# Kernel optimization log

Hardware: AMD Instinct MI355X
Metric: run time of the kernel (lower is better)

## Reference

```python
import jax, jax.numpy as jnp
import numpy as np

UNITS = 256  # LSTM hidden size per source (units=256)

def setup_inputs() -> dict:
    key = jax.random.key(0)
    ks = jax.random.split(key, 7)
    vocab, embed_dim, seq_len, batch, n_cls = 50000, 256, 512, 64, 20
    x = jax.random.randint(ks[0], (batch, seq_len), 0, vocab)
    emb = jax.random.normal(ks[1], (vocab, embed_dim), jnp.float32) * 0.05
    W = jax.random.normal(ks[2], (embed_dim, 4 * UNITS), jnp.float32) * (1.0 / np.sqrt(embed_dim))
    U = jax.random.normal(ks[3], (UNITS, 4 * UNITS), jnp.float32) * (1.0 / np.sqrt(UNITS))
    # keras unit_forget_bias: forget-gate bias = 1, others 0 (gate order i,f,c,o)
    b = jnp.concatenate([jnp.zeros((UNITS,)), jnp.ones((UNITS,)), jnp.zeros((2 * UNITS,))]).astype(jnp.float32)
    Wd = jax.random.normal(ks[4], (UNITS, n_cls), jnp.float32) * (1.0 / np.sqrt(UNITS))
    bd = jnp.zeros((n_cls,), jnp.float32)
    return {"x": x, "emb": emb, "W": W, "U": U, "b": b, "Wd": Wd, "bd": bd}

def reference(x, emb, W, U, b, Wd, bd):
    # Embedding lookup: [B, T] -> [B, T, D]
    e = emb[x]
    B = e.shape[0]
    # Pre-compute input projections for all timesteps (one big GEMM): [B, T, 4H]
    xz = jnp.einsum('btd,dh->bth', e, W) + b
    h0 = jnp.zeros((B, UNITS), e.dtype)
    c0 = jnp.zeros((B, UNITS), e.dtype)

    def step(carry, zt):
        h, c = carry
        z = zt + h @ U  # [B, 4H]
        i, f, g, o = jnp.split(z, 4, axis=-1)
        i = jax.nn.sigmoid(i)
        f = jax.nn.sigmoid(f)
        g = jnp.tanh(g)
        o = jax.nn.sigmoid(o)
        c_new = f * c + i * g
        h_new = o * jnp.tanh(c_new)
        return (h_new, c_new), None

    (h_T, _), _ = jax.lax.scan(step, (h0, c0), jnp.swapaxes(xz, 0, 1))
    logits = h_T @ Wd + bd
    return jax.nn.softmax(logits, axis=-1)
```

## Files before the change

### kernel.cpp

```cpp
#include <hip/hip_runtime.h>
#include <hip/hip_bf16.h>
#include <math.h>


typedef __bf16 bf16_t;
typedef bf16_t bf16x8 __attribute__((ext_vector_type(8)));
typedef bf16_t bf16x4 __attribute__((ext_vector_type(4)));
typedef float  f32x4  __attribute__((ext_vector_type(4)));
typedef unsigned long long u64;

#define T_SZ 512
#define HID 256
#define G4 1024
#define NCLS 20

#define WS_UPACK 0u
#define WS_WPACK (512u * 1024u)
#define WS_HFIN  (1024u * 1024u)
#define WS_EXCH  (1536u * 1024u)
#define WS_XZ    (2u * 1024u * 1024u)

__global__ void pack_weights(const float* __restrict__ W, const float* __restrict__ U,
                             bf16_t* __restrict__ Wp, bf16_t* __restrict__ Up) {
    int tid  = blockIdx.x * blockDim.x + threadIdx.x;
    int j    = tid & 7;
    int lane = (tid >> 3) & 63;
    int ks   = (tid >> 9) & 7;
    int nt   = tid >> 12;
    int row  = ks * 32 + ((lane >> 4) << 3) + j;
    int col  = nt * 16 + (lane & 15);
    Wp[tid] = (bf16_t)W[row * G4 + col];
    Up[tid] = (bf16_t)U[row * G4 + col];
}

__global__ __launch_bounds__(256) void xz_gemm(const int* __restrict__ x,
                                               const float* __restrict__ emb,
                                               const bf16_t* __restrict__ Wp,
                                               const float* __restrict__ bias,
                                               bf16x4* __restrict__ xz2) {
    int nb   = blockIdx.x & 7;
    int t    = blockIdx.x >> 3;
    int w    = threadIdx.x >> 6;
    int lane = threadIdx.x & 63;
    int l15  = lane & 15;
    int quad = lane >> 4;

    int b_row = w * 16 + l15;
    int tok   = x[b_row * T_SZ + t];
    const float* erow = emb + (size_t)tok * 256;

    bf16x8 afrag[8];
#pragma unroll
    for (int ks = 0; ks < 8; ks++) {
        const float4* p = (const float4*)(erow + ks * 32 + quad * 8);
        float4 v0 = p[0], v1 = p[1];
        bf16x8 a;
        a[0] = (bf16_t)v0.x; a[1] = (bf16_t)v0.y; a[2] = (bf16_t)v0.z; a[3] = (bf16_t)v0.w;
        a[4] = (bf16_t)v1.x; a[5] = (bf16_t)v1.y; a[6] = (bf16_t)v1.z; a[7] = (bf16_t)v1.w;
        afrag[ks] = a;
    }

    const bf16x8* Wf = (const bf16x8*)Wp;

#pragma unroll
    for (int nt = 0; nt < 8; nt++) {
        int ntg = nb * 8 + nt;
        float bv = bias[ntg * 16 + l15];
        f32x4 acc = {bv, bv, bv, bv};
        const bf16x8* bp = Wf + (size_t)(ntg * 8) * 64 + lane;
#pragma unroll
        for (int ks = 0; ks < 8; ks++) {
            bf16x8 bfrag = bp[ks * 64];
            acc = __builtin_amdgcn_mfma_f32_16x16x32_bf16(afrag[ks], bfrag, acc, 0, 0, 0);
        }
        bf16x4 hv;
#pragma unroll
        for (int r = 0; r < 4; r++) hv[r] = (bf16_t)acc[r];
        xz2[((size_t)(t * 4 + w) * 64 + ntg) * 64 + lane] = hv;
    }
}

__device__ __forceinline__ float sigmoid_f(float z) {
    return 1.0f / (1.0f + __expf(-z));
}
__device__ __forceinline__ float tanh_f(float z) {
    float e = __expf(2.0f * z);
    return 1.0f - 2.0f / (e + 1.0f);
}
__device__ __forceinline__ unsigned pack2(float a, float b) {
    unsigned short xs = __builtin_bit_cast(unsigned short, (bf16_t)a);
    unsigned short ys = __builtin_bit_cast(unsigned short, (bf16_t)b);
    return (unsigned)xs | ((unsigned)ys << 16);
}
__device__ __forceinline__ bf16_t unpk_lo(unsigned v) {
    return __builtin_bit_cast(bf16_t, (unsigned short)(v & 0xffffu));
}
__device__ __forceinline__ bf16_t unpk_hi(unsigned v) {
    return __builtin_bit_cast(bf16_t, (unsigned short)(v >> 16));
}

__device__ __forceinline__ void mfma_aB(f32x4& d, bf16x8 a, bf16x8 b) {
    asm("v_mfma_f32_16x16x32_bf16 %0, %1, %2, %0" : "+v"(d) : "v"(a), "a"(b));
}

__global__ __launch_bounds__(512, 2) void lstm_pair(const bf16x4* __restrict__ xz2,
                                                    const bf16_t* __restrict__ Up,
                                                    u64* __restrict__ exch,
                                                    float* __restrict__ hfin) {
    if (blockIdx.x & 4) return;
    const int g    = blockIdx.x & 3;
    const int p    = (blockIdx.x >> 3) & 1;
    const int w    = threadIdx.x >> 6;
    const int lane = threadIdx.x & 63;
    const int l15  = lane & 15;
    const int quad = lane >> 4;

    __shared__ __align__(16) bf16_t h_lds[2][16][264];

    const bf16x8* Uf = (const bf16x8*)Up + lane;
    bf16x8 u[4][8];
#pragma unroll
    for (int G = 0; G < 4; G++) {
        int ntg = G * 16 + p * 8 + w;
#pragma unroll
        for (int ks = 0; ks < 8; ks++)
            u[G][ks] = Uf[(ntg * 8 + ks) * 64];
    }
    asm volatile("" : "+a"(u[0][0]), "+a"(u[0][1]), "+a"(u[0][2]), "+a"(u[0][3]),
                      "+a"(u[0][4]), "+a"(u[0][5]), "+a"(u[0][6]), "+a"(u[0][7]));
    asm volatile("" : "+a"(u[1][0]), "+a"(u[1][1]), "+a"(u[1][2]), "+a"(u[1][3]),
                      "+a"(u[1][4]), "+a"(u[1][5]), "+a"(u[1][6]), "+a"(u[1][7]));
    asm volatile("" : "+a"(u[2][0]), "+a"(u[2][1]), "+a"(u[2][2]), "+a"(u[2][3]),
                      "+a"(u[2][4]), "+a"(u[2][5]), "+a"(u[2][6]), "+a"(u[2][7]));
    asm volatile("" : "+a"(u[3][0]), "+a"(u[3][1]), "+a"(u[3][2]), "+a"(u[3][3]),
                      "+a"(u[3][4]), "+a"(u[3][5]), "+a"(u[3][6]), "+a"(u[3][7]));

    for (int i = threadIdx.x; i < 2 * 16 * 264; i += 512)
        (&h_lds[0][0][0])[i] = (bf16_t)0.0f;

    f32x4 cst = {0.f, 0.f, 0.f, 0.f};

    bf16x4 xzv[4];
#pragma unroll
    for (int G = 0; G < 4; G++)
        xzv[G] = xz2[((size_t)(0 * 4 + g) * 64 + (G * 16 + p * 8 + w)) * 64 + lane];

    __syncthreads();

    for (int t = 0; t < T_SZ; t++) {
        const int buf  = t & 1;
        const int nbuf = buf ^ 1;
        const unsigned key = ((unsigned)(t >> 3) + 1u) << 24;

        bf16x8 af[8];
#pragma unroll
        for (int ks = 0; ks < 8; ks++)
            af[ks] = *(const bf16x8*)&h_lds[buf][l15][ks * 32 + quad * 8];

        f32x4 acc[4];
#pragma unroll
        for (int G = 0; G < 4; G++) {
            bf16x4 xv = xzv[G];
            f32x4 a = {(float)xv[0], (float)xv[1], (float)xv[2], (float)xv[3]};
            acc[G] = a;
        }
#pragma unroll
        for (int ks = 0; ks < 8; ks++)
#pragma unroll
            for (int G = 0; G < 4; G++)
                mfma_aB(acc[G], af[ks], u[G][ks]);

        if (t + 1 < T_SZ) {
#pragma unroll
            for (int G = 0; G < 4; G++)
                xzv[G] = xz2[((size_t)((t + 1) * 4 + g) * 64 + (G * 16 + p * 8 + w)) * 64 + lane];
        }

        float hv[4];
#pragma unroll
        for (int r = 0; r < 4; r++) {
            float ig = sigmoid_f(acc[0][r]);
            float fg = sigmoid_f(acc[1][r]);
            float gg = tanh_f(acc[2][r]);
            float og = sigmoid_f(acc[3][r]);
            float cn = fg * cst[r] + ig * gg;
            cst[r] = cn;
            hv[r] = og * tanh_f(cn);
        }

        if (t == T_SZ - 1) {
#pragma unroll
            for (int r = 0; r < 4; r++)
                hfin[(g * 16 + quad * 4 + r) * HID + p * 128 + w * 16 + l15] = hv[r];
            break;
        }

        {
            unsigned dw0 = pack2(hv[0], hv[1]);
            unsigned dw1 = pack2(hv[2], hv[3]);
            u64 q0 = (u64)dw0 | ((u64)(dw0 ^ key) << 32);
            u64 q1 = (u64)dw1 | ((u64)(dw1 ^ key) << 32);
            unsigned base = (((unsigned)(t & 7) * 4 + (unsigned)g) * 2 + (unsigned)p) * 1024u;
            unsigned ui   = (unsigned)(w * 16 + l15) * 8u + (unsigned)(quad * 2);
            __hip_atomic_store(&exch[base + ui],     q0, __ATOMIC_RELAXED, __HIP_MEMORY_SCOPE_AGENT);
            __hip_atomic_store(&exch[base + ui + 1], q1, __ATOMIC_RELAXED, __HIP_MEMORY_SCOPE_AGENT);
        }

#pragma unroll
        for (int r = 0; r < 4; r++)
            h_lds[nbuf][quad * 4 + r][p * 128 + w * 16 + l15] = (bf16_t)hv[r];

        {
            unsigned pbase = (((unsigned)(t & 7) * 4 + (unsigned)g) * 2 + (unsigned)(1 - p)) * 1024u;
            unsigned i0 = (unsigned)threadIdx.x * 2u;
            u64 q0, q1;
            for (;;) {
                q0 = __hip_atomic_load(&exch[pbase + i0],     __ATOMIC_RELAXED, __HIP_MEMORY_SCOPE_AGENT);
                q1 = __hip_atomic_load(&exch[pbase + i0 + 1], __ATOMIC_RELAXED, __HIP_MEMORY_SCOPE_AGENT);
                bool v0 = ((unsigned)(q0 >> 32)) == (((unsigned)q0) ^ key);
                bool v1 = ((unsigned)(q1 >> 32)) == (((unsigned)q1) ^ key);
                if (v0 && v1) break;
            }
            unsigned d0 = (unsigned)q0, d1 = (unsigned)q1;
            int ul  = (int)(i0 >> 3);
            int qq  = (int)((i0 & 7) >> 1);
            int col = (1 - p) * 128 + ul;
            h_lds[nbuf][qq * 4 + 0][col] = unpk_lo(d0);
            h_lds[nbuf][qq * 4 + 1][col] = unpk_hi(d0);
            h_lds[nbuf][qq * 4 + 2][col] = unpk_lo(d1);
            h_lds[nbuf][qq * 4 + 3][col] = unpk_hi(d1);
        }

        __syncthreads();
    }
}

__global__ void head(const float* __restrict__ hfin, const float* __restrict__ Wd,
                     const float* __restrict__ bd, float* __restrict__ out) {
    __shared__ float hrow[HID];
    __shared__ float lg[32];
    __shared__ float ex[32];
    int b = blockIdx.x, tid = threadIdx.x;
    for (int i = tid; i < HID; i += 64) hrow[i] = hfin[b * HID + i];
    __syncthreads();
    if (tid < NCLS) {
        float acc = bd[tid];
        for (int k = 0; k < HID; k++) acc = fmaf(hrow[k], Wd[k * NCLS + tid], acc);
        lg[tid] = acc;
    }
    __syncthreads();
    if (tid < NCLS) {
        float m = -1e30f;
        for (int jj = 0; jj < NCLS; jj++) m = fmaxf(m, lg[jj]);
        ex[tid] = __expf(lg[tid] - m);
    }
    __syncthreads();
    if (tid < NCLS) {
        float sden = 0.0f;
        for (int jj = 0; jj < NCLS; jj++) sden += ex[jj];
        out[b * NCLS + tid] = ex[tid] / sden;
    }
}

extern "C" void kernel_launch(void* const* d_in, const int* in_sizes, int n_in,
                              void* d_out, int out_size, void* d_ws, size_t ws_size,
                              hipStream_t stream) {
    const int*   x    = (const int*)d_in[0];
    const float* emb  = (const float*)d_in[1];
    const float* W    = (const float*)d_in[2];
    const float* U    = (const float*)d_in[3];
    const float* bias = (const float*)d_in[4];
    const float* Wd   = (const float*)d_in[5];
    const float* bd   = (const float*)d_in[6];
    float* out = (float*)d_out;

    char* ws = (char*)d_ws;
    bf16_t* Up   = (bf16_t*)(ws + WS_UPACK);
    bf16_t* Wp   = (bf16_t*)(ws + WS_WPACK);
    float*  hf   = (float*)(ws + WS_HFIN);
    u64*    exch = (u64*)(ws + WS_EXCH);
    bf16x4* xz2  = (bf16x4*)(ws + WS_XZ);

    pack_weights<<<dim3(1024), dim3(256), 0, stream>>>(W, U, Wp, Up);
    xz_gemm<<<dim3(4096), dim3(256), 0, stream>>>(x, emb, Wp, bias, xz2);
    lstm_pair<<<dim3(16), dim3(512), 0, stream>>>(xz2, Up, exch, hf);
    head<<<dim3(64), dim3(64), 0, stream>>>(hf, Wd, bd, out);
}
```

Baseline: 1.458 ms.

## Run each batch group's LSTM on one block, dropping cross-block h exchange

Replaces the two-block-per-batch-group recurrence, which swapped half of h every step through global-memory atomics with spin-wait flags, with a single 512-thread block per group that computes all 256 hidden units. Each wave now owns two column tiles. One tile's U slices stay in AGPRs, half of the other tile's U lives in LDS, and the remaining quarter is streamed from global/L2 every step. This removes the inter-block polling latency from the serial per-step critical path. In exchange each block does twice the MFMA work per step and adds LDS and L2 weight traffic inside the time loop.

```diff
diff --git a/kernel.cpp b/kernel.cpp
--- a/kernel.cpp
+++ b/kernel.cpp
@@ -17,7 +17,6 @@
 #define WS_UPACK 0u
 #define WS_WPACK (512u * 1024u)
 #define WS_HFIN  (1024u * 1024u)
-#define WS_EXCH  (1536u * 1024u)
 #define WS_XZ    (2u * 1024u * 1024u)
 
 __global__ void pack_weights(const float* __restrict__ W, const float* __restrict__ U,
@@ -87,150 +86,181 @@
     float e = __expf(2.0f * z);
     return 1.0f - 2.0f / (e + 1.0f);
 }
-__device__ __forceinline__ unsigned pack2(float a, float b) {
-    unsigned short xs = __builtin_bit_cast(unsigned short, (bf16_t)a);
-    unsigned short ys = __builtin_bit_cast(unsigned short, (bf16_t)b);
-    return (unsigned)xs | ((unsigned)ys << 16);
-}
-__device__ __forceinline__ bf16_t unpk_lo(unsigned v) {
-    return __builtin_bit_cast(bf16_t, (unsigned short)(v & 0xffffu));
-}
-__device__ __forceinline__ bf16_t unpk_hi(unsigned v) {
-    return __builtin_bit_cast(bf16_t, (unsigned short)(v >> 16));
-}
 
 __device__ __forceinline__ void mfma_aB(f32x4& d, bf16x8 a, bf16x8 b) {
     asm("v_mfma_f32_16x16x32_bf16 %0, %1, %2, %0" : "+v"(d) : "v"(a), "a"(b));
 }
 
-__global__ __launch_bounds__(512, 2) void lstm_pair(const bf16x4* __restrict__ xz2,
+__global__ __launch_bounds__(512, 2) void lstm_solo(const bf16x4* __restrict__ xz2,
                                                     const bf16_t* __restrict__ Up,
-                                                    u64* __restrict__ exch,
                                                     float* __restrict__ hfin) {
-    if (blockIdx.x & 4) return;
-    const int g    = blockIdx.x & 3;
-    const int p    = (blockIdx.x >> 3) & 1;
+    __shared__ bf16x8 ulds[128 * 64];
+    __shared__ __align__(16) bf16_t h_lds[2][16][264];
+
+    const int g    = blockIdx.x;
     const int w    = threadIdx.x >> 6;
     const int lane = threadIdx.x & 63;
     const int l15  = lane & 15;
     const int quad = lane >> 4;
-
-    __shared__ __align__(16) bf16_t h_lds[2][16][264];
-
-    const bf16x8* Uf = (const bf16x8*)Up + lane;
-    bf16x8 u[4][8];
-#pragma unroll
-    for (int G = 0; G < 4; G++) {
-        int ntg = G * 16 + p * 8 + w;
+    const int ntA  = 2 * w;
+    const int ntB  = 2 * w + 1;
+
+    const bf16x8* Uf  = (const bf16x8*)Up + lane;
+    const bf16x8* Ufr = (const bf16x8*)Up;
+
+    bf16x8 uA[4][8];
+#pragma unroll
+    for (int G = 0; G < 4; G++)
 #pragma unroll
         for (int ks = 0; ks < 8; ks++)
-            u[G][ks] = Uf[(ntg * 8 + ks) * 64];
-    }
-    asm volatile("" : "+a"(u[0][0]), "+a"(u[0][1]), "+a"(u[0][2]), "+a"(u[0][3]),
-                      "+a"(u[0][4]), "+a"(u[0][5]), "+a"(u[0][6]), "+a"(u[0][7]));
-    asm volatile("" : "+a"(u[1][0]), "+a"(u[1][1]), "+a"(u[1][2]), "+a"(u[1][3]),
-                      "+a"(u[1][4]), "+a"(u[1][5]), "+a"(u[1][6]), "+a"(u[1][7]));
-    asm volatile("" : "+a"(u[2][0]), "+a"(u[2][1]), "+a"(u[2][2]), "+a"(u[2][3]),
-                      "+a"(u[2][4]), "+a"(u[2][5]), "+a"(u[2][6]), "+a"(u[2][7]));
-    asm volatile("" : "+a"(u[3][0]), "+a"(u[3][1]), "+a"(u[3][2]), "+a"(u[3][3]),
-                      "+a"(u[3][4]), "+a"(u[3][5]), "+a"(u[3][6]), "+a"(u[3][7]));
-
+            uA[G][ks] = Uf[((G * 16 + ntA) * 8 + ks) * 64];
+    asm volatile("" : "+a"(uA[0][0]), "+a"(uA[0][1]), "+a"(uA[0][2]), "+a"(uA[0][3]),
+                      "+a"(uA[0][4]), "+a"(uA[0][5]), "+a"(uA[0][6]), "+a"(uA[0][7]));
+    asm volatile("" : "+a"(uA[1][0]), "+a"(uA[1][1]), "+a"(uA[1][2]), "+a"(uA[1][3]),
+                      "+a"(uA[1][4]), "+a"(uA[1][5]), "+a"(uA[1][6]), "+a"(uA[1][7]));
+    asm volatile("" : "+a"(uA[2][0]), "+a"(uA[2][1]), "+a"(uA[2][2]), "+a"(uA[2][3]),
+                      "+a"(uA[2][4]), "+a"(uA[2][5]), "+a"(uA[2][6]), "+a"(uA[2][7]));
+    asm volatile("" : "+a"(uA[3][0]), "+a"(uA[3][1]), "+a"(uA[3][2]), "+a"(uA[3][3]),
+                      "+a"(uA[3][4]), "+a"(uA[3][5]), "+a"(uA[3][6]), "+a"(uA[3][7]));
+
+    for (int i = threadIdx.x; i < 128 * 64; i += 512) {
+        int fi = i >> 6, ln = i & 63;
+        int w2 = fi >> 4, G = (fi >> 2) & 3, ks = fi & 3;
+        ulds[i] = Ufr[((G * 16 + 2 * w2 + 1) * 8 + ks) * 64 + ln];
+    }
     for (int i = threadIdx.x; i < 2 * 16 * 264; i += 512)
         (&h_lds[0][0][0])[i] = (bf16_t)0.0f;
 
-    f32x4 cst = {0.f, 0.f, 0.f, 0.f};
-
-    bf16x4 xzv[4];
-#pragma unroll
-    for (int G = 0; G < 4; G++)
-        xzv[G] = xz2[((size_t)(0 * 4 + g) * 64 + (G * 16 + p * 8 + w)) * 64 + lane];
+    f32x4 cstA = {0.f, 0.f, 0.f, 0.f};
+    f32x4 cstB = {0.f, 0.f, 0.f, 0.f};
+
+    bf16x4 xzvA[4], xzvB[4];
+#pragma unroll
+    for (int G = 0; G < 4; G++) {
+        xzvA[G] = xz2[((size_t)(0 * 4 + g) * 64 + (G * 16 + ntA)) * 64 + lane];
+        xzvB[G] = xz2[((size_t)(0 * 4 + g) * 64 + (G * 16 + ntB)) * 64 + lane];
+    }
 
     __syncthreads();
 
     for (int t = 0; t < T_SZ; t++) {
         const int buf  = t & 1;
         const int nbuf = buf ^ 1;
-        const unsigned key = ((unsigned)(t >> 3) + 1u) << 24;
 
         bf16x8 af[8];
 #pragma unroll
         for (int ks = 0; ks < 8; ks++)
             af[ks] = *(const bf16x8*)&h_lds[buf][l15][ks * 32 + quad * 8];
 
-        f32x4 acc[4];
+        f32x4 aA[4], aB[4];
 #pragma unroll
         for (int G = 0; G < 4; G++) {
-            bf16x4 xv = xzv[G];
-            f32x4 a = {(float)xv[0], (float)xv[1], (float)xv[2], (float)xv[3]};
-            acc[G] = a;
-        }
+            aA[G] = f32x4{(float)xzvA[G][0], (float)xzvA[G][1], (float)xzvA[G][2], (float)xzvA[G][3]};
+            aB[G] = f32x4{(float)xzvB[G][0], (float)xzvB[G][1], (float)xzvB[G][2], (float)xzvB[G][3]};
+        }
+
 #pragma unroll
         for (int ks = 0; ks < 8; ks++)
 #pragma unroll
             for (int G = 0; G < 4; G++)
-                mfma_aB(acc[G], af[ks], u[G][ks]);
+                mfma_aB(aA[G], af[ks], uA[G][ks]);
 
         if (t + 1 < T_SZ) {
 #pragma unroll
-            for (int G = 0; G < 4; G++)
-                xzv[G] = xz2[((size_t)((t + 1) * 4 + g) * 64 + (G * 16 + p * 8 + w)) * 64 + lane];
-        }
-
-        float hv[4];
-#pragma unroll
-        for (int r = 0; r < 4; r++) {
-            float ig = sigmoid_f(acc[0][r]);
-            float fg = sigmoid_f(acc[1][r]);
-            float gg = tanh_f(acc[2][r]);
-            float og = sigmoid_f(acc[3][r]);
-            float cn = fg * cst[r] + ig * gg;
-            cst[r] = cn;
-            hv[r] = og * tanh_f(cn);
-        }
-
-        if (t == T_SZ - 1) {
-#pragma unroll
-            for (int r = 0; r < 4; r++)
-                hfin[(g * 16 + quad * 4 + r) * HID + p * 128 + w * 16 + l15] = hv[r];
-            break;
+            for (int G = 0; G < 4; G++) {
+                xzvA[G] = xz2[((size_t)((t + 1) * 4 + g) * 64 + (G * 16 + ntA)) * 64 + lane];
+                xzvB[G] = xz2[((size_t)((t + 1) * 4 + g) * 64 + (G * 16 + ntB)) * 64 + lane];
+            }
         }
 
         {
-            unsigned dw0 = pack2(hv[0], hv[1]);
-            unsigned dw1 = pack2(hv[2], hv[3]);
-            u64 q0 = (u64)dw0 | ((u64)(dw0 ^ key) << 32);
-            u64 q1 = (u64)dw1 | ((u64)(dw1 ^ key) << 32);
-            unsigned base = (((unsigned)(t & 7) * 4 + (unsigned)g) * 2 + (unsigned)p) * 1024u;
-            unsigned ui   = (unsigned)(w * 16 + l15) * 8u + (unsigned)(quad * 2);
-            __hip_atomic_store(&exch[base + ui],     q0, __ATOMIC_RELAXED, __HIP_MEMORY_SCOPE_AGENT);
-            __hip_atomic_store(&exch[base + ui + 1], q1, __ATOMIC_RELAXED, __HIP_MEMORY_SCOPE_AGENT);
-        }
-
-#pragma unroll
-        for (int r = 0; r < 4; r++)
-            h_lds[nbuf][quad * 4 + r][p * 128 + w * 16 + l15] = (bf16_t)hv[r];
+            float hv[4];
+#pragma unroll
+            for (int r = 0; r < 4; r++) {
+                float ig = sigmoid_f(aA[0][r]);
+                float fg = sigmoid_f(aA[1][r]);
+                float gg = tanh_f(aA[2][r]);
+                float og = sigmoid_f(aA[3][r]);
+                float cn = fg * cstA[r] + ig * gg;
+                cstA[r] = cn;
+                hv[r] = og * tanh_f(cn);
+            }
+            if (t == T_SZ - 1) {
+#pragma unroll
+                for (int r = 0; r < 4; r++)
+                    hfin[(g * 16 + quad * 4 + r) * HID + 32 * w + l15] = hv[r];
+            } else {
+#pragma unroll
+                for (int r = 0; r < 4; r++)
+                    h_lds[nbuf][quad * 4 + r][32 * w + l15] = (bf16_t)hv[r];
+            }
+        }
+
+        uintptr_t pU = (uintptr_t)Up;
+        asm volatile("" : "+v"(pU));
+        const bf16x8* Ufs = (const bf16x8*)pU + lane;
+
+        bf16x8 s0[4], s1[4];
+#pragma unroll
+        for (int j = 0; j < 4; j++) s0[j] = Ufs[((0 * 16 + ntB) * 8 + 4 + j) * 64];
+#pragma unroll
+        for (int j = 0; j < 4; j++) s1[j] = Ufs[((1 * 16 + ntB) * 8 + 4 + j) * 64];
+
+        unsigned uo = 0;
+        asm volatile("" : "+v"(uo));
+        const bf16x8* ub = ulds + ((unsigned)(w * 16) << 6) + lane + uo;
+#pragma unroll
+        for (int ks = 0; ks < 4; ks++)
+#pragma unroll
+            for (int G = 0; G < 4; G++) {
+                bf16x8 bfrag = ub[(unsigned)((G * 4 + ks) << 6)];
+                aB[G] = __builtin_amdgcn_mfma_f32_16x16x32_bf16(af[ks], bfrag, aB[G], 0, 0, 0);
+            }
+
+        bf16x8 s2[4];
+#pragma unroll
+        for (int j = 0; j < 4; j++) s2[j] = Ufs[((2 * 16 + ntB) * 8 + 4 + j) * 64];
+#pragma unroll
+        for (int j = 0; j < 4; j++)
+            aB[0] = __builtin_amdgcn_mfma_f32_16x16x32_bf16(af[4 + j], s0[j], aB[0], 0, 0, 0);
+
+        bf16x8 s3[4];
+#pragma unroll
+        for (int j = 0; j < 4; j++) s3[j] = Ufs[((3 * 16 + ntB) * 8 + 4 + j) * 64];
+#pragma unroll
+        for (int j = 0; j < 4; j++)
+            aB[1] = __builtin_amdgcn_mfma_f32_16x16x32_bf16(af[4 + j], s1[j], aB[1], 0, 0, 0);
+#pragma unroll
+        for (int j = 0; j < 4; j++)
+            aB[2] = __builtin_amdgcn_mfma_f32_16x16x32_bf16(af[4 + j], s2[j], aB[2], 0, 0, 0);
+#pragma unroll
+        for (int j = 0; j < 4; j++)
+            aB[3] = __builtin_amdgcn_mfma_f32_16x16x32_bf16(af[4 + j], s3[j], aB[3], 0, 0, 0);
 
         {
-            unsigned pbase = (((unsigned)(t & 7) * 4 + (unsigned)g) * 2 + (unsigned)(1 - p)) * 1024u;
-            unsigned i0 = (unsigned)threadIdx.x * 2u;
-            u64 q0, q1;
-            for (;;) {
-                q0 = __hip_atomic_load(&exch[pbase + i0],     __ATOMIC_RELAXED, __HIP_MEMORY_SCOPE_AGENT);
-                q1 = __hip_atomic_load(&exch[pbase + i0 + 1], __ATOMIC_RELAXED, __HIP_MEMORY_SCOPE_AGENT);
-                bool v0 = ((unsigned)(q0 >> 32)) == (((unsigned)q0) ^ key);
-                bool v1 = ((unsigned)(q1 >> 32)) == (((unsigned)q1) ^ key);
-                if (v0 && v1) break;
-            }
-            unsigned d0 = (unsigned)q0, d1 = (unsigned)q1;
-            int ul  = (int)(i0 >> 3);
-            int qq  = (int)((i0 & 7) >> 1);
-            int col = (1 - p) * 128 + ul;
-            h_lds[nbuf][qq * 4 + 0][col] = unpk_lo(d0);
-            h_lds[nbuf][qq * 4 + 1][col] = unpk_hi(d0);
-            h_lds[nbuf][qq * 4 + 2][col] = unpk_lo(d1);
-            h_lds[nbuf][qq * 4 + 3][col] = unpk_hi(d1);
-        }
-
+            float hv[4];
+#pragma unroll
+            for (int r = 0; r < 4; r++) {
+                float ig = sigmoid_f(aB[0][r]);
+                float fg = sigmoid_f(aB[1][r]);
+                float gg = tanh_f(aB[2][r]);
+                float og = sigmoid_f(aB[3][r]);
+                float cn = fg * cstB[r] + ig * gg;
+                cstB[r] = cn;
+                hv[r] = og * tanh_f(cn);
+            }
+            if (t == T_SZ - 1) {
+#pragma unroll
+                for (int r = 0; r < 4; r++)
+                    hfin[(g * 16 + quad * 4 + r) * HID + 32 * w + 16 + l15] = hv[r];
+            } else {
+#pragma unroll
+                for (int r = 0; r < 4; r++)
+                    h_lds[nbuf][quad * 4 + r][32 * w + 16 + l15] = (bf16_t)hv[r];
+            }
+        }
+
+        if (t == T_SZ - 1) break;
         __syncthreads();
     }
 }
@@ -275,14 +305,13 @@
     float* out = (float*)d_out;
 
     char* ws = (char*)d_ws;
-    bf16_t* Up   = (bf16_t*)(ws + WS_UPACK);
-    bf16_t* Wp   = (bf16_t*)(ws + WS_WPACK);
-    float*  hf   = (float*)(ws + WS_HFIN);
-    u64*    exch = (u64*)(ws + WS_EXCH);
-    bf16x4* xz2  = (bf16x4*)(ws + WS_XZ);
+    bf16_t* Up  = (bf16_t*)(ws + WS_UPACK);
+    bf16_t* Wp  = (bf16_t*)(ws + WS_WPACK);
+    float*  hf  = (float*)(ws + WS_HFIN);
+    bf16x4* xz2 = (bf16x4*)(ws + WS_XZ);
 
     pack_weights<<<dim3(1024), dim3(256), 0, stream>>>(W, U, Wp, Up);
     xz_gemm<<<dim3(4096), dim3(256), 0, stream>>>(x, emb, Wp, bias, xz2);
-    lstm_pair<<<dim3(16), dim3(512), 0, stream>>>(xz2, Up, exch, hf);
+    lstm_solo<<<dim3(4), dim3(512), 0, stream>>>(xz2, Up, hf);
     head<<<dim3(64), dim3(64), 0, stream>>>(hf, Wd, bd, out);
 }
```

New measurement: 3.048 ms. +109.0%, slower.
